# Kernel tuning notes

Measured on AMD Instinct MI355X. Metric: run time of the kernel, lower is better.

Reference implementation:

```python
import jax, jax.numpy as jnp
import numpy as np

V, E, H, B, S, C = 50000, 300, 512, 128, 80, 6
HH = 2 * H  # hidden_dim * num_directions (BiDi=True)


def _gru_dir(x, w_ih, w_hh, b_ih, b_hh, reverse):
    # x: (b, t, e) -> (b, t, h); torch nn.GRU cell math
    Bv, T, _ = x.shape
    Hd = w_hh.shape[1]
    xg = jnp.einsum('bte,ge->btg', x, w_ih) + b_ih  # (b, t, 3h)
    if reverse:
        xg = xg[:, ::-1]
    def step(h, xt):
        gi_r, gi_z, gi_n = jnp.split(xt, 3, axis=-1)
        gh_r, gh_z, gh_n = jnp.split(h @ w_hh.T + b_hh, 3, axis=-1)
        r = jax.nn.sigmoid(gi_r + gh_r)
        z = jax.nn.sigmoid(gi_z + gh_z)
        n = jnp.tanh(gi_n + r * gh_n)
        hn = (1.0 - z) * n + z * h
        return hn, hn
    h0 = jnp.zeros((Bv, Hd), x.dtype)
    _, hs = jax.lax.scan(step, h0, jnp.swapaxes(xg, 0, 1))
    hs = jnp.swapaxes(hs, 0, 1)
    if reverse:
        hs = hs[:, ::-1]
    return hs


def _bigru(x, pf, pb):
    return jnp.concatenate([_gru_dir(x, *pf, reverse=False), _gru_dir(x, *pb, reverse=True)], axis=-1)


def _conv1d(x, w, b, d):
    y = jax.lax.conv_general_dilated(x, w, (1,), 'VALID', rhs_dilation=(d,),
                                     dimension_numbers=('NCH', 'OIH', 'NCH'))
    return y + b[None, :, None]


def _bn(x, g, b, m, v):
    # eval-mode BatchNorm1d with running stats
    return (x - m[None, :, None]) * (g[None, :, None] / jnp.sqrt(v[None, :, None] + 1e-5)) + b[None, :, None]


def setup_inputs():
    key = jax.random.key(0)
    ks = iter(jax.random.split(key, 64))
    def W(*shape):
        return jax.random.normal(next(ks), shape, jnp.float32) * 0.02
    inp = {
        'input_batch': jax.random.randint(next(ks), (B, S), 1, V),
        'choices_batch': jax.random.randint(next(ks), (B, 4, C), 1, V),
        'emb_table': W(V, E),
    }
    for p in ('sg', 'cg'):
        for d in ('f', 'b'):
            inp[p + '_wih_' + d] = W(3 * H, E)
            inp[p + '_whh_' + d] = W(3 * H, H)
            inp[p + '_bih_' + d] = W(3 * H)
            inp[p + '_bhh_' + d] = W(3 * H)
    inp['lin_w'] = W(HH, HH * C)
    inp['lin_b'] = W(HH)
    inp['attn_w'] = W(HH, HH)
    inp['attn_b'] = W(HH)
    inp['c11_w'] = W(HH, S, 3);  inp['c11_b'] = W(HH)
    inp['c13_w'] = W(HH, HH, 3); inp['c13_b'] = W(HH)
    inp['c21_w'] = W(HH, HH, 3); inp['c21_b'] = W(HH)
    inp['c23_w'] = W(HH, HH, 3); inp['c23_b'] = W(HH)
    for i in ('1', '2'):
        inp['bn' + i + '_g'] = jnp.ones((HH,), jnp.float32)
        inp['bn' + i + '_b'] = jnp.zeros((HH,), jnp.float32)
        inp['bn' + i + '_m'] = jnp.zeros((HH,), jnp.float32)
        inp['bn' + i + '_v'] = jnp.ones((HH,), jnp.float32)
    inp['gate_wp'] = W(2 * HH, HH)
    inp['gate_wc'] = W(2 * HH, 2 * HH)
    inp['gate_b'] = W(2 * HH)
    inp['out_wp'] = W(2 * HH, HH)
    inp['out_b'] = W(2 * HH)
    return inp


def reference(input_batch, choices_batch, emb_table,
              sg_wih_f, sg_whh_f, sg_bih_f, sg_bhh_f, sg_wih_b, sg_whh_b, sg_bih_b, sg_bhh_b,
              cg_wih_f, cg_whh_f, cg_bih_f, cg_bhh_f, cg_wih_b, cg_whh_b, cg_bih_b, cg_bhh_b,
              lin_w, lin_b, attn_w, attn_b,
              c11_w, c11_b, c13_w, c13_b, c21_w, c21_b, c23_w, c23_b,
              bn1_g, bn1_b, bn1_m, bn1_v, bn2_g, bn2_b, bn2_m, bn2_v,
              gate_wp, gate_wc, gate_b, out_wp, out_b):
    # --- encode passage: embedding + BiGRU (dropout is eval-mode identity) ---
    sent = _bigru(emb_table[input_batch],
                  (sg_wih_f, sg_whh_f, sg_bih_f, sg_bhh_f),
                  (sg_wih_b, sg_whh_b, sg_bih_b, sg_bhh_b))  # (B, S, 2h)
    cgf = (cg_wih_f, cg_whh_f, cg_bih_f, cg_bhh_f)
    cgb = (cg_wih_b, cg_whh_b, cg_bih_b, cg_bhh_b)

    def choice_vec(tok):  # (B, C) -> (B, 2h)
        g = _bigru(emb_table[tok], cgf, cgb)               # (B, C, 2h)
        return g.reshape(g.shape[0], -1) @ lin_w.T + lin_b

    cvs = [choice_vec(choices_batch[:, i]) for i in range(4)]

    # --- AttnReader: shared Wh/bh, per-choice softmax attention over seq ---
    Wh = jnp.einsum('bsh,hg->bsg', sent, attn_w)  # (B, S, 2h)
    bh = sent @ attn_b                            # (B, S)

    def attn_read(cv):
        a = jax.nn.softmax(jnp.einsum('bsg,bg->bs', Wh, cv) + bh, axis=1)
        return jnp.einsum('bs,bsh->bh', a, sent)  # (B, 2h)

    pars = [attn_read(cv) for cv in cvs]

    # --- IDCNN: Conv1d treats seq dim S as channels (faithful to source) ---
    x = jax.nn.relu(_bn(_conv1d(sent, c11_w, c11_b, 1), bn1_g, bn1_b, bn1_m, bn1_v))
    x = _conv1d(x, c13_w, c13_b, 3)
    x = jax.nn.relu(_bn(_conv1d(x, c21_w, c21_b, 1), bn2_g, bn2_b, bn2_m, bn2_v))
    x = _conv1d(x, c23_w, c23_b, 3)
    P = jnp.max(x, axis=2)  # AdaptiveMaxPool1d(1) + squeeze -> (B, 2h)

    Cs = [jnp.concatenate([cv, par], axis=1) for cv, par in zip(cvs, pars)]  # (B, 4h)

    # --- PointerNet (note: source bug makes out1..out4 all equal C1WP+bC1) ---
    WP = P @ gate_wp.T          # (B, 4h)
    WP_out = P @ out_wp.T       # (B, 4h)
    Cd1 = Cs[0] * jax.nn.sigmoid(WP + Cs[0] @ gate_wc.T + gate_b)
    o1 = jnp.sum(Cd1 * WP_out, axis=1, keepdims=True) + (Cd1 @ out_b)[:, None]  # (B, 1)
    return jnp.concatenate([o1, o1, o1, o1], axis=1)  # (B, 4)
```

## Files before the change

kernel.cpp:

```cpp
#include <hip/hip_runtime.h>

typedef unsigned int u32;
typedef unsigned short u16;
typedef __attribute__((ext_vector_type(4))) float f32x4;
typedef __attribute__((ext_vector_type(8))) short bf16x8;

#define DEV static __device__ __forceinline__

DEV float sigf(float x){ return 1.0f/(1.0f + expf(-x)); }

DEV u16 f2bf(float x){
  u32 u = __float_as_uint(x);
  u32 r = (u + 0x7FFFu + ((u >> 16) & 1u)) >> 16;
  return (u16)r;
}

DEV u32 encf(float f){
  u32 u = __float_as_uint(f);
  return (u & 0x80000000u) ? ~u : (u | 0x80000000u);
}
DEV float decf(u32 e){
  return (e & 0x80000000u) ? __uint_as_float(e ^ 0x80000000u) : __uint_as_float(~e);
}

DEV void gload16(const void* g, void* l){
  __builtin_amdgcn_global_load_lds((const __attribute__((address_space(1))) u32*)g,
                                   (__attribute__((address_space(3))) u32*)l, 16, 0, 0);
}

__global__ __launch_bounds__(256,2) void gemm_bf16(
    const u16* __restrict__ A, const u16* __restrict__ A2,
    const u16* __restrict__ B,
    const float* __restrict__ bias, const float* __restrict__ bias2,
    float* __restrict__ C, float* __restrict__ C2, int ldc,
    int Kp, int ksteps)
{
  __shared__ u16 lds[(128 + 128)*32];
  char* ldsc = (char*)&lds[0];
  const int Boff = 128*64;
  const int tid = threadIdx.x;
  const int l = tid & 63, w = tid >> 6;
  const int n0 = blockIdx.x * 128, m0 = blockIdx.y * 128;
  const u16* Ause = blockIdx.z ? A2 : A;
  const float* buse = blockIdx.z ? bias2 : bias;
  float* Cuse = blockIdx.z ? C2 : C;
  const int wr = w >> 1, wc = w & 1;
  const int lr = l & 15, g = l >> 4;

  f32x4 acc[4][4];
  #pragma unroll
  for (int i=0;i<4;++i)
    #pragma unroll
    for (int j=0;j<4;++j) acc[i][j] = f32x4{0.f,0.f,0.f,0.f};

  for (int ks = 0; ks < ksteps; ++ks) {
    const int i0 = ks*32;
    __syncthreads();
    #pragma unroll
    for (int r = 0; r < 2; ++r) {
      const int rr = w*2 + r;
      const int c = rr*64 + l;
      const int row = c >> 2, bpos = c & 3;
      const int ib = bpos ^ (row & 3);
      gload16(Ause + ((size_t)(m0 + row)*Kp + (i0 + ib*8)), ldsc + rr*1024);
      gload16(B    + ((size_t)(n0 + row)*Kp + (i0 + ib*8)), ldsc + Boff + rr*1024);
    }
    __syncthreads();
    bf16x8 af[4], bfr[4];
    #pragma unroll
    for (int m=0;m<4;++m){
      int o = wr*64 + m*16 + lr;
      af[m] = *(const bf16x8*)(ldsc + o*64 + ((g ^ (o&3))<<4));
    }
    #pragma unroll
    for (int n=0;n<4;++n){
      int pr = wc*64 + n*16 + lr;
      bfr[n] = *(const bf16x8*)(ldsc + Boff + pr*64 + ((g ^ (pr&3))<<4));
    }
    #pragma unroll
    for (int m=0;m<4;++m)
      #pragma unroll
      for (int n=0;n<4;++n)
        acc[m][n] = __builtin_amdgcn_mfma_f32_16x16x32_bf16(af[m], bfr[n], acc[m][n], 0,0,0);
  }

  #pragma unroll
  for (int m=0;m<4;++m){
    int mm = m0 + wr*64 + m*16 + g*4;
    f32x4 bv = *(const f32x4*)(buse + mm);
    #pragma unroll
    for (int n=0;n<4;++n){
      int p = n0 + wc*64 + n*16 + lr;
      f32x4 v;
      #pragma unroll
      for (int r2=0;r2<4;++r2) v[r2] = acc[m][n][r2] + bv[r2];
      *(f32x4*)(Cuse + (size_t)p*ldc + mm) = v;
    }
  }
}

__global__ __launch_bounds__(256,2) void gemm_bf16_sk(
    const u16* __restrict__ A, const u16* __restrict__ B,
    float* __restrict__ C, int ldc, int Kp, int kpc)
{
  __shared__ u16 lds[(128 + 128)*32];
  char* ldsc = (char*)&lds[0];
  const int Boff = 128*64;
  const int tid = threadIdx.x;
  const int l = tid & 63, w = tid >> 6;
  const int n0 = blockIdx.x * 128, m0 = blockIdx.y * 128;
  const int ks0 = blockIdx.z * kpc;
  const int wr = w >> 1, wc = w & 1;
  const int lr = l & 15, g = l >> 4;

  f32x4 acc[4][4];
  #pragma unroll
  for (int i=0;i<4;++i)
    #pragma unroll
    for (int j=0;j<4;++j) acc[i][j] = f32x4{0.f,0.f,0.f,0.f};

  for (int ks = 0; ks < kpc; ++ks) {
    const int i0 = (ks0 + ks)*32;
    __syncthreads();
    #pragma unroll
    for (int r = 0; r < 2; ++r) {
      const int rr = w*2 + r;
      const int c = rr*64 + l;
      const int row = c >> 2, bpos = c & 3;
      const int ib = bpos ^ (row & 3);
      gload16(A + ((size_t)(m0 + row)*Kp + (i0 + ib*8)), ldsc + rr*1024);
      gload16(B + ((size_t)(n0 + row)*Kp + (i0 + ib*8)), ldsc + Boff + rr*1024);
    }
    __syncthreads();
    bf16x8 af[4], bfr[4];
    #pragma unroll
    for (int m=0;m<4;++m){
      int o = wr*64 + m*16 + lr;
      af[m] = *(const bf16x8*)(ldsc + o*64 + ((g ^ (o&3))<<4));
    }
    #pragma unroll
    for (int n=0;n<4;++n){
      int pr = wc*64 + n*16 + lr;
      bfr[n] = *(const bf16x8*)(ldsc + Boff + pr*64 + ((g ^ (pr&3))<<4));
    }
    #pragma unroll
    for (int m=0;m<4;++m)
      #pragma unroll
      for (int n=0;n<4;++n)
        acc[m][n] = __builtin_amdgcn_mfma_f32_16x16x32_bf16(af[m], bfr[n], acc[m][n], 0,0,0);
  }

  #pragma unroll
  for (int m=0;m<4;++m){
    int mm = m0 + wr*64 + m*16 + g*4;
    #pragma unroll
    for (int n=0;n<4;++n){
      int p = n0 + wc*64 + n*16 + lr;
      float* dst = C + (size_t)p*ldc + mm;
      #pragma unroll
      for (int r2=0;r2<4;++r2) atomicAdd(dst + r2, acc[m][n][r2]);
    }
  }
}

__global__ void initc(float* __restrict__ C, const float* __restrict__ bias,
                      int total, int mmask)
{
  int i = blockIdx.x*256 + threadIdx.x;
  if (i < total) C[i] = bias ? bias[i & mmask] : 0.f;
}

__global__ __launch_bounds__(256) void gru_step(
    const float* __restrict__ xg0, const float* __restrict__ xg1,
    const float* __restrict__ whh0, const float* __restrict__ whh1,
    const float* __restrict__ bhh0, const float* __restrict__ bhh1,
    float* __restrict__ hs, int S, int t)
{
  __shared__ float hL[32*520];
  __shared__ float wL[48*132];
  const int tid = threadIdx.x;
  const int tj = tid & 15, tb = tid >> 4;
  const int jg = blockIdx.x;
  const int b0 = blockIdx.y*32;
  const int dir = blockIdx.z;
  const int l = tid & 63, w = tid >> 6;
  const float* xg  = dir ? xg1  : xg0;
  const float* whh = dir ? whh1 : whh0;
  const float* bhh = dir ? bhh1 : bhh0;
  const int tt = dir ? (S-1-t) : t;
  const int j = jg*16 + tj;

  float accr[2], accz[2], accn[2];
  {
    float br = bhh[j], bz = bhh[512+j], bn = bhh[1024+j];
    accr[0]=br; accr[1]=br; accz[0]=bz; accz[1]=bz; accn[0]=bn; accn[1]=bn;
  }

  if (t > 0){
    const int tp = dir ? (tt+1) : (tt-1);
    #pragma unroll
    for (int rr = 0; rr < 8; ++rr){
      int row = w*8 + rr;
      const float* srcb = hs + ((size_t)(b0+row)*S + tp)*1024 + dir*512;
      gload16(srcb + l*4,       (char*)hL + (size_t)(row*520)*4);
      gload16(srcb + 256 + l*4, (char*)hL + (size_t)(row*520 + 256)*4);
    }
    for (int c = 0; c < 4; ++c){
      const int k0 = c*128;
      __syncthreads();
      #pragma unroll
      for (int i = 0; i < 6; ++i){
        int qidx = tid + i*256;
        int row = qidx >> 5, q = qidx & 31;
        int grow = (row>>4)*512 + jg*16 + (row & 15);
        f32x4 v = *(const f32x4*)(whh + (size_t)grow*512 + k0 + q*4);
        *(f32x4*)(wL + row*132 + q*4) = v;
      }
      __syncthreads();
      #pragma unroll 4
      for (int q = 0; q < 32; ++q){
        f32x4 ha  = *(const f32x4*)(hL + (2*tb  )*520 + k0 + q*4);
        f32x4 hb  = *(const f32x4*)(hL + (2*tb+1)*520 + k0 + q*4);
        f32x4 wr4 = *(const f32x4*)(wL + tj*132      + q*4);
        f32x4 wz4 = *(const f32x4*)(wL + (16+tj)*132 + q*4);
        f32x4 wn4 = *(const f32x4*)(wL + (32+tj)*132 + q*4);
        #pragma unroll
        for (int e = 0; e < 4; ++e){
          accr[0] += ha[e]*wr4[e]; accz[0] += ha[e]*wz4[e]; accn[0] += ha[e]*wn4[e];
          accr[1] += hb[e]*wr4[e]; accz[1] += hb[e]*wz4[e]; accn[1] += hb[e]*wn4[e];
        }
      }
    }
  }

  #pragma unroll
  for (int bi = 0; bi < 2; ++bi){
    int lb = 2*tb + bi;
    int b = b0 + lb;
    size_t xbase = ((size_t)b*S + tt)*1536;
    float gir = xg[xbase + j], giz = xg[xbase + 512 + j], gin = xg[xbase + 1024 + j];
    float hp = (t>0) ? hL[lb*520 + j] : 0.f;
    float r = sigf(gir + accr[bi]);
    float z = sigf(giz + accz[bi]);
    float n = tanhf(gin + r*accn[bi]);
    hs[((size_t)b*S + tt)*1024 + dir*512 + j] = (1.f - z)*n + z*hp;
  }
}

__global__ void transpose_sent(const float* __restrict__ sent, u16* __restrict__ sentT)
{
  __shared__ float tl[80][65];
  int b = blockIdx.y, h0 = blockIdx.x*64;
  for (int idx = threadIdx.x; idx < 80*64; idx += 256){
    int s = idx >> 6, hh = idx & 63;
    tl[s][hh] = sent[((size_t)b*80 + s)*1024 + h0 + hh];
  }
  __syncthreads();
  for (int idx = threadIdx.x; idx < 64*96; idx += 256){
    int hh = idx / 96, s = idx % 96;
    sentT[((size_t)b*1024 + h0 + hh)*96 + s] = (s < 80) ? f2bf(tl[s][hh]) : (u16)0;
  }
}

__global__ void attn_scores(const float* __restrict__ sent, const float* __restrict__ u,
                            const float* __restrict__ attn_b, float* __restrict__ sc)
{
  int wid = blockIdx.x*4 + (threadIdx.x >> 6);
  int lane = threadIdx.x & 63;
  const float* row = sent + (size_t)wid*1024;
  const float* ub = u + (size_t)(wid/80)*1024;
  float acc = 0.f;
  for (int h = lane; h < 1024; h += 64) acc += row[h]*(ub[h] + attn_b[h]);
  #pragma unroll
  for (int m = 32; m; m >>= 1) acc += __shfl_xor(acc, m);
  if (lane == 0) sc[wid] = acc;
}

__global__ void softmax80(const float* __restrict__ sc, float* __restrict__ a)
{
  __shared__ float sv[80];
  __shared__ float inv;
  int b = blockIdx.x, t = threadIdx.x;
  if (t < 80) sv[t] = sc[b*80 + t];
  __syncthreads();
  if (t == 0){
    float mx = -1e30f;
    for (int s = 0; s < 80; ++s) mx = fmaxf(mx, sv[s]);
    float sum = 0.f;
    for (int s = 0; s < 80; ++s){ float e = expf(sv[s]-mx); sv[s] = e; sum += e; }
    inv = 1.f/sum;
  }
  __syncthreads();
  if (t < 80) a[b*80 + t] = sv[t]*inv;
}

__global__ void par_cs0(const float* __restrict__ a, const float* __restrict__ sent,
                        const float* __restrict__ cv, float* __restrict__ Cs0)
{
  int b = blockIdx.x;
  for (int h = threadIdx.x; h < 1024; h += 256){
    float acc = 0.f;
    for (int s = 0; s < 80; ++s) acc += a[b*80+s]*sent[((size_t)b*80+s)*1024 + h];
    Cs0[(size_t)b*2048 + 1024 + h] = acc;
    Cs0[(size_t)b*2048 + h] = cv[(size_t)b*1024 + h];
  }
}

__global__ void pack_w(const float* __restrict__ src, u16* __restrict__ dst,
                       int O, int CIs, int CIp)
{
  int i = blockIdx.x*256 + threadIdx.x;
  int total = 3*O*CIp;
  if (i >= total) return;
  int tap = i/(O*CIp); int rem = i%(O*CIp); int o = rem/CIp, ci = rem%CIp;
  float v = (ci < CIs) ? src[((size_t)o*CIs + ci)*3 + tap] : 0.f;
  dst[((size_t)tap*O + o)*CIp + ci] = f2bf(v);
}

__global__ void pack_wk(const float* __restrict__ src, u16* __restrict__ dst,
                        int M, int Ks, int Kp)
{
  int i = blockIdx.x*256 + threadIdx.x;
  if (i >= M*Kp) return;
  int row = i/Kp, k = i%Kp;
  dst[i] = (k < Ks) ? f2bf(src[(size_t)row*Ks + k]) : (u16)0;
}

__global__ void pack_f2b(const float* __restrict__ src, u16* __restrict__ dst, int n)
{
  int i = blockIdx.x*256 + threadIdx.x;
  if (i < n) dst[i] = f2bf(src[i]);
}

__global__ void pack_x(const float* __restrict__ emb, const int* __restrict__ toks,
                       int rdiv, int rmul, u16* __restrict__ dst, int R)
{
  int i = blockIdx.x*256 + threadIdx.x;
  if (i >= R*320) return;
  int row = i/320, k = i%320;
  int tok = toks[(row/rdiv)*rmul + (row%rdiv)];
  dst[i] = (k < 300) ? f2bf(emb[(size_t)tok*300 + k]) : (u16)0;
}

__global__ void prep_ab(const float* c11b, const float* c13b, const float* c21b, const float* c23b,
                        const float* g1, const float* b1, const float* m1, const float* v1,
                        const float* g2, const float* b2, const float* m2, const float* v2,
                        float* ab)
{
  int i = blockIdx.x*256 + threadIdx.x;
  if (i >= 4096) return;
  int layer = i >> 10, o = i & 1023;
  float al, be;
  if (layer == 0){ al = g1[o]/sqrtf(v1[o]+1e-5f); be = c11b[o]*al + b1[o] - m1[o]*al; }
  else if (layer == 1){ al = 1.f; be = c13b[o]; }
  else if (layer == 2){ al = g2[o]/sqrtf(v2[o]+1e-5f); be = c21b[o]*al + b2[o] - m2[o]*al; }
  else { al = 1.f; be = c23b[o]; }
  ab[layer*2048 + o] = al;
  ab[layer*2048 + 1024 + o] = be;
}

__global__ void init_penc(u32* p){
  int i = blockIdx.x*256 + threadIdx.x;
  if (i < 128*1024) p[i] = encf(-3.3e38f);
}
__global__ void dec_p(const u32* __restrict__ pe, float* __restrict__ pf){
  int i = blockIdx.x*256 + threadIdx.x;
  if (i < 128*1024) pf[i] = decf(pe[i]);
}

__global__ __launch_bounds__(512,4) void conv_mfma(
    const u16* __restrict__ X, long bstrideX,
    const u16* __restrict__ Wt,
    const float* __restrict__ alpha, const float* __restrict__ beta,
    u16* __restrict__ Y, long bstrideY,
    u32* __restrict__ Penc, int b0,
    int P_in, int P_out, int CI, int dil, int ksteps, int mode)
{
  __shared__ u16 lds[(384 + 272)*32];
  char* ldsc = (char*)&lds[0];
  const int Boff = 384*64;
  const int tid = threadIdx.x;
  const int l = tid & 63, w = tid >> 6;
  const int p0 = blockIdx.x * 256, o0 = blockIdx.y * 128;
  const int bz = blockIdx.z;
  const u16* Xb = X + (size_t)bz * (size_t)bstrideX;
  const int wr = w >> 2, wc = w & 3;
  const int lr = l & 15, g = l >> 4;

  f32x4 acc[4][4];
  #pragma unroll
  for (int i=0;i<4;++i)
    #pragma unroll
    for (int j=0;j<4;++j) acc[i][j] = f32x4{0.f,0.f,0.f,0.f};

  for (int ks = 0; ks < ksteps; ++ks) {
    const int i0 = ks*32;
    __syncthreads();
    #pragma unroll
    for (int r = 0; r < 3; ++r) {
      const int c = r*512 + tid;
      const int row = c >> 2, bpos = c & 3;
      const int tap = row >> 7, o = row & 127;
      const int ib = bpos ^ (o & 3);
      gload16(Wt + ((size_t)(tap*1024 + o0 + o)*CI + (i0 + ib*8)), ldsc + (size_t)c*16);
    }
    #pragma unroll
    for (int r = 0; r < 3; ++r) {
      const int c = r*512 + tid;
      if (c < 1088){
        const int row = c >> 2, bpos = c & 3;
        const int ib = bpos ^ (row & 3);
        int ps = p0 + row; ps = ps < P_in ? ps : (P_in - 1);
        gload16(Xb + ((size_t)ps*CI + (i0 + ib*8)), ldsc + Boff + (size_t)c*16);
      }
    }
    __syncthreads();
    #pragma unroll
    for (int tap = 0; tap < 3; ++tap) {
      bf16x8 af[4], bfr[4];
      #pragma unroll
      for (int m=0;m<4;++m){
        int o = wr*64 + m*16 + lr;
        af[m] = *(const bf16x8*)(ldsc + (tap*128 + o)*64 + ((g ^ (o&3))<<4));
      }
      #pragma unroll
      for (int n=0;n<4;++n){
        int pr = wc*64 + n*16 + lr + dil*tap;
        bfr[n] = *(const bf16x8*)(ldsc + Boff + pr*64 + ((g ^ (pr&3))<<4));
      }
      #pragma unroll
      for (int m=0;m<4;++m)
        #pragma unroll
        for (int n=0;n<4;++n)
          acc[m][n] = __builtin_amdgcn_mfma_f32_16x16x32_bf16(af[m], bfr[n], acc[m][n], 0,0,0);
    }
  }

  if (mode == 2) {
    #pragma unroll
    for (int m=0;m<4;++m){
      int oo = o0 + wr*64 + m*16 + g*4;
      f32x4 al = *(const f32x4*)(alpha + oo);
      f32x4 be = *(const f32x4*)(beta + oo);
      float vm[4] = {-1e30f,-1e30f,-1e30f,-1e30f};
      #pragma unroll
      for (int n=0;n<4;++n){
        int p = p0 + wc*64 + n*16 + lr;
        bool ok = p < P_out;
        #pragma unroll
        for (int r2=0;r2<4;++r2){
          float v = acc[m][n][r2]*al[r2] + be[r2];
          vm[r2] = ok ? fmaxf(vm[r2], v) : vm[r2];
        }
      }
      #pragma unroll
      for (int r2=0;r2<4;++r2){
        float v = vm[r2];
        #pragma unroll
        for (int mask=1; mask<16; mask<<=1) v = fmaxf(v, __shfl_xor(v, mask));
        if (lr == 0) atomicMax(&Penc[(size_t)(b0+bz)*1024 + oo + r2], encf(v));
      }
    }
  } else {
    #pragma unroll
    for (int m=0;m<4;++m){
      int oo = o0 + wr*64 + m*16 + g*4;
      f32x4 al = *(const f32x4*)(alpha + oo);
      f32x4 be = *(const f32x4*)(beta + oo);
      #pragma unroll
      for (int n=0;n<4;++n){
        int p = p0 + wc*64 + n*16 + lr;
        if (p < P_out){
          float v0 = acc[m][n][0]*al[0] + be[0];
          float v1 = acc[m][n][1]*al[1] + be[1];
          float v2 = acc[m][n][2]*al[2] + be[2];
          float v3 = acc[m][n][3]*al[3] + be[3];
          if (mode == 0){ v0=fmaxf(v0,0.f); v1=fmaxf(v1,0.f); v2=fmaxf(v2,0.f); v3=fmaxf(v3,0.f); }
          uint2 pk;
          pk.x = (u32)f2bf(v0) | ((u32)f2bf(v1) << 16);
          pk.y = (u32)f2bf(v2) | ((u32)f2bf(v3) << 16);
          *(uint2*)(Y + (size_t)bz*(size_t)bstrideY + (size_t)p*1024 + oo) = pk;
        }
      }
    }
  }
}

__global__ void head_final(const float* __restrict__ Cs0, const float* __restrict__ t1,
                           const float* __restrict__ t2, const float* __restrict__ outb,
                           float* __restrict__ dout)
{
  __shared__ float red[256];
  int b = blockIdx.x;
  float part = 0.f;
  for (int gg = threadIdx.x; gg < 2048; gg += 256){
    float cd = Cs0[(size_t)b*2048+gg] * sigf(t1[(size_t)b*2048+gg]);
    part += cd * (t2[(size_t)b*2048+gg] + outb[gg]);
  }
  red[threadIdx.x] = part;
  __syncthreads();
  for (int s = 128; s > 0; s >>= 1){
    if (threadIdx.x < s) red[threadIdx.x] += red[threadIdx.x + s];
    __syncthreads();
  }
  if (threadIdx.x < 4) dout[b*4 + threadIdx.x] = red[0];
}

extern "C" void kernel_launch(void* const* d_in, const int* in_sizes, int n_in,
                              void* d_out, int out_size, void* d_ws, size_t ws_size,
                              hipStream_t stream)
{
  (void)in_sizes; (void)n_in; (void)out_size; (void)ws_size;
  const int*   input_batch = (const int*)d_in[0];
  const int*   choices     = (const int*)d_in[1];
  const float* emb    = (const float*)d_in[2];
  const float* sgwihf = (const float*)d_in[3];
  const float* sgwhhf = (const float*)d_in[4];
  const float* sgbihf = (const float*)d_in[5];
  const float* sgbhhf = (const float*)d_in[6];
  const float* sgwihb = (const float*)d_in[7];
  const float* sgwhhb = (const float*)d_in[8];
  const float* sgbihb = (const float*)d_in[9];
  const float* sgbhhb = (const float*)d_in[10];
  const float* cgwihf = (const float*)d_in[11];
  const float* cgwhhf = (const float*)d_in[12];
  const float* cgbihf = (const float*)d_in[13];
  const float* cgbhhf = (const float*)d_in[14];
  const float* cgwihb = (const float*)d_in[15];
  const float* cgwhhb = (const float*)d_in[16];
  const float* cgbihb = (const float*)d_in[17];
  const float* cgbhhb = (const float*)d_in[18];
  const float* lin_w  = (const float*)d_in[19];
  const float* lin_b  = (const float*)d_in[20];
  const float* attn_w = (const float*)d_in[21];
  const float* attn_b = (const float*)d_in[22];
  const float* c11w = (const float*)d_in[23];
  const float* c11b = (const float*)d_in[24];
  const float* c13w = (const float*)d_in[25];
  const float* c13b = (const float*)d_in[26];
  const float* c21w = (const float*)d_in[27];
  const float* c21b = (const float*)d_in[28];
  const float* c23w = (const float*)d_in[29];
  const float* c23b = (const float*)d_in[30];
  const float* bn1g = (const float*)d_in[31];
  const float* bn1b = (const float*)d_in[32];
  const float* bn1m = (const float*)d_in[33];
  const float* bn1v = (const float*)d_in[34];
  const float* bn2g = (const float*)d_in[35];
  const float* bn2b = (const float*)d_in[36];
  const float* bn2m = (const float*)d_in[37];
  const float* bn2v = (const float*)d_in[38];
  const float* gatewp = (const float*)d_in[39];
  const float* gatewc = (const float*)d_in[40];
  const float* gateb  = (const float*)d_in[41];
  const float* outwp  = (const float*)d_in[42];
  const float* outb   = (const float*)d_in[43];
  float* dout = (float*)d_out;

  char* ws = (char*)d_ws; size_t off = 0;
  auto alc = [&](size_t n)->char*{ char* p = ws + off; off = (off + n + 255) & ~(size_t)255; return p; };
  float* xg_f  = (float*)alc((size_t)128*80*1536*4);
  float* xg_b  = (float*)alc((size_t)128*80*1536*4);
  float* xg_cf = (float*)alc((size_t)128*6*1536*4);
  float* xg_cb = (float*)alc((size_t)128*6*1536*4);
  float* gh    = (float*)alc((size_t)2*128*1536*4); (void)gh;
  float* sent  = (float*)alc((size_t)128*80*1024*4);
  float* g_c   = (float*)alc((size_t)128*6*1024*4);
  u16*   sentT = (u16*)alc((size_t)128*1024*96*2);
  float* cv    = (float*)alc((size_t)128*1024*4);
  float* uu    = (float*)alc((size_t)128*1024*4);
  float* scb   = (float*)alc((size_t)128*80*4);
  float* aw    = (float*)alc((size_t)128*80*4);
  float* Cs0   = (float*)alc((size_t)128*2048*4);
  u16* W1p = (u16*)alc((size_t)3*1024*96*2);
  u16* W2p = (u16*)alc((size_t)3*1024*1024*2);
  u16* W3p = (u16*)alc((size_t)3*1024*1024*2);
  u16* W4p = (u16*)alc((size_t)3*1024*1024*2);
  float* ab  = (float*)alc((size_t)4*2048*4);
  u32*  Penc = (u32*)alc((size_t)128*1024*4);
  float* Pf  = (float*)alc((size_t)128*1024*4);
  float* t1  = (float*)alc((size_t)128*2048*4);
  float* t2  = (float*)alc((size_t)128*2048*4);
  u16* xbf_s = (u16*)alc((size_t)10240*320*2);
  u16* xbf_c = (u16*)alc((size_t)768*320*2);
  u16* Wsf = (u16*)alc((size_t)1536*320*2);
  u16* Wsb = (u16*)alc((size_t)1536*320*2);
  u16* Wcf = (u16*)alc((size_t)1536*320*2);
  u16* Wcb = (u16*)alc((size_t)1536*320*2);

  char* R1 = (char*)xg_f;
  u16* linw_bf  = (u16*)(R1);
  u16* attnw_bf = (u16*)(R1 + 12582912);
  u16* gcbf     = (u16*)(R1 + 14680064);
  u16* cvbf     = (u16*)(R1 + 16252928);
  const int bc = 16;
  u16* Y0 = (u16*)(R1 + 16515072);
  u16* Y1 = Y0 + (size_t)bc*1024*1024;
  char* R2 = (char*)sent;
  u16* gwp_bf = (u16*)(R2);
  u16* gwc_bf = (u16*)(R2 + 4194304);
  u16* owp_bf = (u16*)(R2 + 12582912);
  u16* Pfbf   = (u16*)(R2 + 16777216);
  u16* Cs0bf  = (u16*)(R2 + 17039360);

  dim3 T(256), T5(512);

  pack_w<<<dim3((3*1024*96+255)/256), T, 0, stream>>>(c11w, W1p, 1024, 80, 96);
  pack_w<<<dim3((3*1024*1024+255)/256), T, 0, stream>>>(c13w, W2p, 1024, 1024, 1024);
  pack_w<<<dim3((3*1024*1024+255)/256), T, 0, stream>>>(c21w, W3p, 1024, 1024, 1024);
  pack_w<<<dim3((3*1024*1024+255)/256), T, 0, stream>>>(c23w, W4p, 1024, 1024, 1024);
  pack_wk<<<dim3((1536*320+255)/256), T, 0, stream>>>(sgwihf, Wsf, 1536, 300, 320);
  pack_wk<<<dim3((1536*320+255)/256), T, 0, stream>>>(sgwihb, Wsb, 1536, 300, 320);
  pack_wk<<<dim3((1536*320+255)/256), T, 0, stream>>>(cgwihf, Wcf, 1536, 300, 320);
  pack_wk<<<dim3((1536*320+255)/256), T, 0, stream>>>(cgwihb, Wcb, 1536, 300, 320);
  pack_x<<<dim3((10240*320+255)/256), T, 0, stream>>>(emb, input_batch, 80, 80, xbf_s, 10240);
  pack_x<<<dim3((768*320+255)/256), T, 0, stream>>>(emb, choices, 6, 24, xbf_c, 768);
  prep_ab<<<16, T, 0, stream>>>(c11b, c13b, c21b, c23b,
                                bn1g,bn1b,bn1m,bn1v, bn2g,bn2b,bn2m,bn2v, ab);
  init_penc<<<512, T, 0, stream>>>(Penc);

  gemm_bf16<<<dim3(80,12,2), T, 0, stream>>>(Wsf, Wsb, xbf_s, sgbihf, sgbihb,
                                             xg_f, xg_b, 1536, 320, 10);
  gemm_bf16<<<dim3(6,12,2), T, 0, stream>>>(Wcf, Wcb, xbf_c, cgbihf, cgbihb,
                                            xg_cf, xg_cb, 1536, 320, 10);

  for (int t = 0; t < 80; ++t)
    gru_step<<<dim3(32,4,2), T, 0, stream>>>(xg_f, xg_b, sgwhhf, sgwhhb,
                                             sgbhhf, sgbhhb, sent, 80, t);
  for (int t = 0; t < 6; ++t)
    gru_step<<<dim3(32,4,2), T, 0, stream>>>(xg_cf, xg_cb, cgwhhf, cgwhhb,
                                             cgbhhf, cgbhhb, g_c, 6, t);

  pack_wk<<<dim3((1024*6144+255)/256), T, 0, stream>>>(lin_w, linw_bf, 1024, 6144, 6144);
  pack_wk<<<dim3((1024*1024+255)/256), T, 0, stream>>>(attn_w, attnw_bf, 1024, 1024, 1024);
  pack_f2b<<<dim3((128*6144+255)/256), T, 0, stream>>>(g_c, gcbf, 128*6144);

  transpose_sent<<<dim3(16,128), T, 0, stream>>>(sent, sentT);

  initc<<<dim3((128*1024+255)/256), T, 0, stream>>>(cv, lin_b, 128*1024, 1023);
  gemm_bf16_sk<<<dim3(1,8,6), T, 0, stream>>>(linw_bf, gcbf, cv, 1024, 6144, 32);
  pack_f2b<<<dim3((128*1024+255)/256), T, 0, stream>>>(cv, cvbf, 128*1024);
  initc<<<dim3((128*1024+255)/256), T, 0, stream>>>(uu, nullptr, 128*1024, 1023);
  gemm_bf16_sk<<<dim3(1,8,2), T, 0, stream>>>(attnw_bf, cvbf, uu, 1024, 1024, 16);
  attn_scores<<<2560, T, 0, stream>>>(sent, uu, attn_b, scb);
  softmax80<<<128, dim3(128), 0, stream>>>(scb, aw);
  par_cs0<<<128, T, 0, stream>>>(aw, sent, cv, Cs0);

  pack_wk<<<dim3((2048*1024+255)/256), T, 0, stream>>>(gatewp, gwp_bf, 2048, 1024, 1024);
  pack_wk<<<dim3((2048*2048+255)/256), T, 0, stream>>>(gatewc, gwc_bf, 2048, 2048, 2048);
  pack_wk<<<dim3((2048*1024+255)/256), T, 0, stream>>>(outwp, owp_bf, 2048, 1024, 1024);
  pack_f2b<<<dim3((128*2048+255)/256), T, 0, stream>>>(Cs0, Cs0bf, 128*2048);

  for (int b0 = 0; b0 < 128; b0 += bc){
    conv_mfma<<<dim3(4,8,bc), T5, 0, stream>>>(sentT + (size_t)b0*1024*96, (long)1024*96,
        W1p, ab+0,    ab+1024, Y0, (long)1024*1024, nullptr, 0, 1024, 1022, 96,   1, 3,  0);
    conv_mfma<<<dim3(4,8,bc), T5, 0, stream>>>(Y0, (long)1024*1024,
        W2p, ab+2048, ab+3072, Y1, (long)1024*1024, nullptr, 0, 1022, 1016, 1024, 3, 32, 1);
    conv_mfma<<<dim3(4,8,bc), T5, 0, stream>>>(Y1, (long)1024*1024,
        W3p, ab+4096, ab+5120, Y0, (long)1024*1024, nullptr, 0, 1016, 1014, 1024, 1, 32, 0);
    conv_mfma<<<dim3(4,8,bc), T5, 0, stream>>>(Y0, (long)1024*1024,
        W4p, ab+6144, ab+7168, nullptr, 0, Penc, b0,          1014, 1008, 1024, 3, 32, 2);
  }
  dec_p<<<512, T, 0, stream>>>(Penc, Pf);
  pack_f2b<<<dim3((128*1024+255)/256), T, 0, stream>>>(Pf, Pfbf, 128*1024);

  initc<<<dim3((128*2048+255)/256), T, 0, stream>>>(t1, gateb, 128*2048, 2047);
  gemm_bf16_sk<<<dim3(1,16,2), T, 0, stream>>>(gwp_bf, Pfbf, t1, 2048, 1024, 16);
  gemm_bf16_sk<<<dim3(1,16,4), T, 0, stream>>>(gwc_bf, Cs0bf, t1, 2048, 2048, 16);
  initc<<<dim3((128*2048+255)/256), T, 0, stream>>>(t2, nullptr, 128*2048, 2047);
  gemm_bf16_sk<<<dim3(1,16,2), T, 0, stream>>>(owp_bf, Pfbf, t2, 2048, 1024, 16);
  head_final<<<128, T, 0, stream>>>(Cs0, t1, t2, outb, dout);
}
```

Before: 3.994 ms.

## Use 4-wave conv blocks with 64x128 warp tiles and a new LDS swizzle

The conv kernel drops from 8 waves per 512-thread block to 4 waves per 256-thread block. Each wave now computes a 64x128 output tile with 32 accumulators, loads each B fragment once and reuses it across four MFMAs, so fewer LDS reads are needed per MFMA. The LDS XOR swizzle in the conv and both GEMM kernels changes from row&3 to (row>>1)&3 to cut bank conflicts on 16-byte fragment reads. In exchange each thread holds more accumulator registers, which with launch bounds of 256,2 may lower occupancy.

```diff
diff --git a/kernel.cpp b/kernel.cpp
--- a/kernel.cpp
+++ b/kernel.cpp
@@ -61,7 +61,7 @@
       const int rr = w*2 + r;
       const int c = rr*64 + l;
       const int row = c >> 2, bpos = c & 3;
-      const int ib = bpos ^ (row & 3);
+      const int ib = bpos ^ ((row>>1) & 3);
       gload16(Ause + ((size_t)(m0 + row)*Kp + (i0 + ib*8)), ldsc + rr*1024);
       gload16(B    + ((size_t)(n0 + row)*Kp + (i0 + ib*8)), ldsc + Boff + rr*1024);
     }
@@ -70,12 +70,12 @@
     #pragma unroll
     for (int m=0;m<4;++m){
       int o = wr*64 + m*16 + lr;
-      af[m] = *(const bf16x8*)(ldsc + o*64 + ((g ^ (o&3))<<4));
+      af[m] = *(const bf16x8*)(ldsc + o*64 + ((g ^ ((o>>1)&3))<<4));
     }
     #pragma unroll
     for (int n=0;n<4;++n){
       int pr = wc*64 + n*16 + lr;
-      bfr[n] = *(const bf16x8*)(ldsc + Boff + pr*64 + ((g ^ (pr&3))<<4));
+      bfr[n] = *(const bf16x8*)(ldsc + Boff + pr*64 + ((g ^ ((pr>>1)&3))<<4));
     }
     #pragma unroll
     for (int m=0;m<4;++m)
@@ -127,7 +127,7 @@
       const int rr = w*2 + r;
       const int c = rr*64 + l;
       const int row = c >> 2, bpos = c & 3;
-      const int ib = bpos ^ (row & 3);
+      const int ib = bpos ^ ((row>>1) & 3);
       gload16(A + ((size_t)(m0 + row)*Kp + (i0 + ib*8)), ldsc + rr*1024);
       gload16(B + ((size_t)(n0 + row)*Kp + (i0 + ib*8)), ldsc + Boff + rr*1024);
     }
@@ -136,12 +136,12 @@
     #pragma unroll
     for (int m=0;m<4;++m){
       int o = wr*64 + m*16 + lr;
-      af[m] = *(const bf16x8*)(ldsc + o*64 + ((g ^ (o&3))<<4));
+      af[m] = *(const bf16x8*)(ldsc + o*64 + ((g ^ ((o>>1)&3))<<4));
     }
     #pragma unroll
     for (int n=0;n<4;++n){
       int pr = wc*64 + n*16 + lr;
-      bfr[n] = *(const bf16x8*)(ldsc + Boff + pr*64 + ((g ^ (pr&3))<<4));
+      bfr[n] = *(const bf16x8*)(ldsc + Boff + pr*64 + ((g ^ ((pr>>1)&3))<<4));
     }
     #pragma unroll
     for (int m=0;m<4;++m)
@@ -368,7 +368,7 @@
   if (i < 128*1024) pf[i] = decf(pe[i]);
 }
 
-__global__ __launch_bounds__(512,4) void conv_mfma(
+__global__ __launch_bounds__(256,2) void conv_mfma(
     const u16* __restrict__ X, long bstrideX,
     const u16* __restrict__ Wt,
     const float* __restrict__ alpha, const float* __restrict__ beta,
@@ -384,32 +384,32 @@
   const int p0 = blockIdx.x * 256, o0 = blockIdx.y * 128;
   const int bz = blockIdx.z;
   const u16* Xb = X + (size_t)bz * (size_t)bstrideX;
-  const int wr = w >> 2, wc = w & 3;
+  const int wr = w >> 1, wc = w & 1;
   const int lr = l & 15, g = l >> 4;
 
-  f32x4 acc[4][4];
+  f32x4 acc[4][8];
   #pragma unroll
   for (int i=0;i<4;++i)
     #pragma unroll
-    for (int j=0;j<4;++j) acc[i][j] = f32x4{0.f,0.f,0.f,0.f};
+    for (int j=0;j<8;++j) acc[i][j] = f32x4{0.f,0.f,0.f,0.f};
 
   for (int ks = 0; ks < ksteps; ++ks) {
     const int i0 = ks*32;
     __syncthreads();
     #pragma unroll
-    for (int r = 0; r < 3; ++r) {
-      const int c = r*512 + tid;
+    for (int r = 0; r < 6; ++r) {
+      const int c = r*256 + tid;
       const int row = c >> 2, bpos = c & 3;
       const int tap = row >> 7, o = row & 127;
-      const int ib = bpos ^ (o & 3);
+      const int ib = bpos ^ ((o>>1) & 3);
       gload16(Wt + ((size_t)(tap*1024 + o0 + o)*CI + (i0 + ib*8)), ldsc + (size_t)c*16);
     }
     #pragma unroll
-    for (int r = 0; r < 3; ++r) {
-      const int c = r*512 + tid;
+    for (int r = 0; r < 5; ++r) {
+      const int c = r*256 + tid;
       if (c < 1088){
         const int row = c >> 2, bpos = c & 3;
-        const int ib = bpos ^ (row & 3);
+        const int ib = bpos ^ ((row>>1) & 3);
         int ps = p0 + row; ps = ps < P_in ? ps : (P_in - 1);
         gload16(Xb + ((size_t)ps*CI + (i0 + ib*8)), ldsc + Boff + (size_t)c*16);
       }
@@ -417,22 +417,20 @@
     __syncthreads();
     #pragma unroll
     for (int tap = 0; tap < 3; ++tap) {
-      bf16x8 af[4], bfr[4];
+      bf16x8 af[4];
       #pragma unroll
       for (int m=0;m<4;++m){
         int o = wr*64 + m*16 + lr;
-        af[m] = *(const bf16x8*)(ldsc + (tap*128 + o)*64 + ((g ^ (o&3))<<4));
-      }
-      #pragma unroll
-      for (int n=0;n<4;++n){
-        int pr = wc*64 + n*16 + lr + dil*tap;
-        bfr[n] = *(const bf16x8*)(ldsc + Boff + pr*64 + ((g ^ (pr&3))<<4));
-      }
-      #pragma unroll
-      for (int m=0;m<4;++m)
+        af[m] = *(const bf16x8*)(ldsc + (tap*128 + o)*64 + ((g ^ ((o>>1)&3))<<4));
+      }
+      #pragma unroll
+      for (int n=0;n<8;++n){
+        int pr = wc*128 + n*16 + lr + dil*tap;
+        bf16x8 bfr = *(const bf16x8*)(ldsc + Boff + pr*64 + ((g ^ ((pr>>1)&3))<<4));
         #pragma unroll
-        for (int n=0;n<4;++n)
-          acc[m][n] = __builtin_amdgcn_mfma_f32_16x16x32_bf16(af[m], bfr[n], acc[m][n], 0,0,0);
+        for (int m=0;m<4;++m)
+          acc[m][n] = __builtin_amdgcn_mfma_f32_16x16x32_bf16(af[m], bfr, acc[m][n], 0,0,0);
+      }
     }
   }
 
@@ -444,8 +442,8 @@
       f32x4 be = *(const f32x4*)(beta + oo);
       float vm[4] = {-1e30f,-1e30f,-1e30f,-1e30f};
       #pragma unroll
-      for (int n=0;n<4;++n){
-        int p = p0 + wc*64 + n*16 + lr;
+      for (int n=0;n<8;++n){
+        int p = p0 + wc*128 + n*16 + lr;
         bool ok = p < P_out;
         #pragma unroll
         for (int r2=0;r2<4;++r2){
@@ -468,8 +466,8 @@
       f32x4 al = *(const f32x4*)(alpha + oo);
       f32x4 be = *(const f32x4*)(beta + oo);
       #pragma unroll
-      for (int n=0;n<4;++n){
-        int p = p0 + wc*64 + n*16 + lr;
+      for (int n=0;n<8;++n){
+        int p = p0 + wc*128 + n*16 + lr;
         if (p < P_out){
           float v0 = acc[m][n][0]*al[0] + be[0];
           float v1 = acc[m][n][1]*al[1] + be[1];
@@ -603,7 +601,7 @@
   u16* Pfbf   = (u16*)(R2 + 16777216);
   u16* Cs0bf  = (u16*)(R2 + 17039360);
 
-  dim3 T(256), T5(512);
+  dim3 T(256);
 
   pack_w<<<dim3((3*1024*96+255)/256), T, 0, stream>>>(c11w, W1p, 1024, 80, 96);
   pack_w<<<dim3((3*1024*1024+255)/256), T, 0, stream>>>(c13w, W2p, 1024, 1024, 1024);
@@ -652,13 +650,13 @@
   pack_f2b<<<dim3((128*2048+255)/256), T, 0, stream>>>(Cs0, Cs0bf, 128*2048);
 
   for (int b0 = 0; b0 < 128; b0 += bc){
-    conv_mfma<<<dim3(4,8,bc), T5, 0, stream>>>(sentT + (size_t)b0*1024*96, (long)1024*96,
+    conv_mfma<<<dim3(4,8,bc), T, 0, stream>>>(sentT + (size_t)b0*1024*96, (long)1024*96,
         W1p, ab+0,    ab+1024, Y0, (long)1024*1024, nullptr, 0, 1024, 1022, 96,   1, 3,  0);
-    conv_mfma<<<dim3(4,8,bc), T5, 0, stream>>>(Y0, (long)1024*1024,
+    conv_mfma<<<dim3(4,8,bc), T, 0, stream>>>(Y0, (long)1024*1024,
         W2p, ab+2048, ab+3072, Y1, (long)1024*1024, nullptr, 0, 1022, 1016, 1024, 3, 32, 1);
-    conv_mfma<<<dim3(4,8,bc), T5, 0, stream>>>(Y1, (long)1024*1024,
+    conv_mfma<<<dim3(4,8,bc), T, 0, stream>>>(Y1, (long)1024*1024,
         W3p, ab+4096, ab+5120, Y0, (long)1024*1024, nullptr, 0, 1016, 1014, 1024, 1, 32, 0);
-    conv_mfma<<<dim3(4,8,bc), T5, 0, stream>>>(Y0, (long)1024*1024,
+    conv_mfma<<<dim3(4,8,bc), T, 0, stream>>>(Y0, (long)1024*1024,
         W4p, ab+6144, ab+7168, nullptr, 0, Penc, b0,          1014, 1008, 1024, 3, 32, 2);
   }
   dec_p<<<512, T, 0, stream>>>(Penc, Pf);
```

After: 3.935 ms. No clear change (-1.5%).
